# Performance work log

Hardware: AMD Instinct MI355X
Metric: run time of the kernel (lower is better)

## Reference

```python
import jax, jax.numpy as jnp
import numpy as np

EMBED_DIM = 1024
NUM_HEADS = 16
HEAD_DIM = EMBED_DIM // NUM_HEADS


def setup_inputs() -> dict:
    key = jax.random.key(0)
    k1, k2, k3, k4, k5 = jax.random.split(key, 5)
    x = jax.random.normal(k1, (4, 2048, EMBED_DIM), dtype=jnp.float32)
    # nn.Linear params: weight [out, in], bias [out]
    s_in = 1.0 / np.sqrt(EMBED_DIM)
    W_qkv = jax.random.uniform(k2, (3 * EMBED_DIM, EMBED_DIM), jnp.float32, -s_in, s_in)
    b_qkv = jax.random.uniform(k3, (3 * EMBED_DIM,), jnp.float32, -s_in, s_in)
    W_out = jax.random.uniform(k4, (EMBED_DIM, EMBED_DIM), jnp.float32, -s_in, s_in)
    b_out = jax.random.uniform(k5, (EMBED_DIM,), jnp.float32, -s_in, s_in)
    return {"x": x, "W_qkv": W_qkv, "b_qkv": b_qkv, "W_out": W_out, "b_out": b_out}


def reference(x, W_qkv, b_qkv, W_out, b_out):
    B, S, D = x.shape
    H, Dh = NUM_HEADS, HEAD_DIM
    qkv = x @ W_qkv.T + b_qkv                      # [B, S, 3D]
    qkv = qkv.reshape(B, S, 3, H, Dh)
    q = qkv[:, :, 0].transpose(0, 2, 1, 3)        # [B, H, S, Dh]
    k = qkv[:, :, 1].transpose(0, 2, 1, 3)
    v = qkv[:, :, 2].transpose(0, 2, 1, 3)
    scale = 1.0 / jnp.sqrt(jnp.asarray(Dh, x.dtype))
    scores = jnp.einsum('bhqd,bhkd->bhqk', q, k) * scale  # [B, H, S, S]
    attn = jax.nn.softmax(scores, axis=-1)
    out = jnp.einsum('bhqk,bhkd->bhqd', attn, v)  # [B, H, S, Dh]
    out = out.transpose(0, 2, 1, 3).reshape(B, S, D)
    return out @ W_out.T + b_out
```

## Files before the change

kernel.cpp:

```cpp
#include <hip/hip_runtime.h>

#define BB 4
#define SS 2048
#define DD 1024
#define HH 16
#define DHH 64
#define MM (BB*SS)

typedef __bf16 bf16x8 __attribute__((ext_vector_type(8)));
typedef __bf16 bf16x4 __attribute__((ext_vector_type(4)));
typedef float  f32x4  __attribute__((ext_vector_type(4)));
typedef float  f32x16 __attribute__((ext_vector_type(16)));
typedef unsigned int u32;
typedef unsigned int u32x4 __attribute__((ext_vector_type(4)));

__device__ __forceinline__ unsigned short f2bf(float x) {
    unsigned int u = __float_as_uint(x);
    u += 0x7FFFu + ((u >> 16) & 1u);
    return (unsigned short)(u >> 16);
}

__device__ __forceinline__ void glds16(const __bf16* g, __bf16* l) {
    __builtin_amdgcn_global_load_lds(
        (const __attribute__((address_space(1))) void*)g,
        (__attribute__((address_space(3))) void*)l, 16, 0, 0);
}

__global__ __launch_bounds__(256) void cvt_all(
    const float4* __restrict__ x,  const float4* __restrict__ wq,
    const float4* __restrict__ wo,
    ushort4* __restrict__ xb, ushort4* __restrict__ wqb, ushort4* __restrict__ wob)
{
    int i = blockIdx.x * 256 + threadIdx.x;
    const float4* src; ushort4* dst; int j;
    if (i < 2097152)      { src = x;  dst = xb;  j = i; }
    else if (i < 2883584) { src = wq; dst = wqb; j = i - 2097152; }
    else                  { src = wo; dst = wob; j = i - 2883584; }
    float4 v = src[j];
    ushort4 o;
    o.x = f2bf(v.x); o.y = f2bf(v.y); o.z = f2bf(v.z); o.w = f2bf(v.w);
    dst[j] = o;
}

__global__ __launch_bounds__(256) void qkv_gemm(
    const __bf16* __restrict__ A,
    const __bf16* __restrict__ W,
    const float* __restrict__ bias,
    __bf16* __restrict__ Qp,
    __bf16* __restrict__ Kp,
    __bf16* __restrict__ Vp)
{
    __shared__ __bf16 smem[16896];
#define CT(r,c) smem[(r)*132 + (c)]
    __bf16* As = smem;
    __bf16* Bs = smem + 8192;
    const int tid  = threadIdx.x;
    const int m0   = blockIdx.x * 128;
    const int n0   = blockIdx.y * 128;
    const int lane = tid & 63;
    const int wid  = tid >> 6;
    const int fr   = lane & 15;
    const int quad = lane >> 4;
    const int wm   = (wid >> 1) * 64;
    const int wn   = (wid & 1) * 64;

    const int srow = lane >> 3;
    const int sg   = ((lane & 7) - srow) & 7;

    f32x4 acc[4][4] = {};

    for (int k0 = 0; k0 < DD; k0 += 64) {
        __syncthreads();
        #pragma unroll
        for (int p = 0; p < 4; ++p) {
            int cidx = p * 4 + wid;
            int r = cidx * 8 + srow;
            glds16(A + (size_t)(m0 + r) * DD + k0 + sg * 8, As + cidx * 512);
            glds16(W + (size_t)(n0 + r) * DD + k0 + sg * 8, Bs + cidx * 512);
        }
        __syncthreads();

        bf16x8 af[2][4], bw[2][4];
        #pragma unroll
        for (int kc = 0; kc < 2; ++kc)
            #pragma unroll
            for (int t = 0; t < 4; ++t) {
                int col = ((kc * 4 + quad + fr) & 7) * 8;
                af[kc][t] = *(const bf16x8*)&As[(wm + t*16 + fr) * 64 + col];
                bw[kc][t] = *(const bf16x8*)&Bs[(wn + t*16 + fr) * 64 + col];
            }
        #pragma unroll
        for (int kc = 0; kc < 2; ++kc)
            #pragma unroll
            for (int mt = 0; mt < 4; ++mt)
                #pragma unroll
                for (int nt = 0; nt < 4; ++nt)
                    acc[mt][nt] = __builtin_amdgcn_mfma_f32_16x16x32_bf16(
                        af[kc][mt], bw[kc][nt], acc[mt][nt], 0, 0, 0);
    }

    __syncthreads();
    const int t3 = n0 >> 10;
    const int b  = m0 >> 11;
    const int s0 = m0 & (SS - 1);

    float bn[4];
    #pragma unroll
    for (int nt = 0; nt < 4; ++nt) bn[nt] = bias[n0 + wn + nt*16 + fr];

    if (t3 == 2) {
        #pragma unroll
        for (int nt = 0; nt < 4; ++nt)
            #pragma unroll
            for (int mt = 0; mt < 4; ++mt) {
                f32x4 t;
                #pragma unroll
                for (int i = 0; i < 4; ++i) t[i] = acc[mt][nt][i] + bn[nt];
                *(bf16x4*)&CT(wn + nt*16 + fr, wm + mt*16 + quad*4) =
                    __builtin_convertvector(t, bf16x4);
            }
        __syncthreads();
        const int pn0 = n0 - 2048;
        #pragma unroll
        for (int p = 0; p < 8; ++p) {
            int g = tid + p * 256;
            int r = g >> 4;
            int c = (g & 15) << 3;
            int pn = pn0 + r, h = pn >> 6, dh = pn & 63;
            *(uint4*)&Vp[((size_t)((b*HH + h)*DHH + dh))*SS + s0 + c] = *(uint4*)&CT(r, c);
        }
    } else {
        __bf16* dst = (t3 == 0) ? Qp : Kp;
        const float qscale = (t3 == 0) ? 0.125f * 1.44269504088896340736f : 1.0f;
        #pragma unroll
        for (int nt = 0; nt < 4; ++nt)
            #pragma unroll
            for (int mt = 0; mt < 4; ++mt)
                #pragma unroll
                for (int i = 0; i < 4; ++i)
                    CT(wm + mt*16 + quad*4 + i, wn + nt*16 + fr) =
                        (__bf16)((acc[mt][nt][i] + bn[nt]) * qscale);
        __syncthreads();
        const int pn0 = (t3 == 0) ? n0 : n0 - 1024;
        #pragma unroll
        for (int p = 0; p < 8; ++p) {
            int g = tid + p * 256;
            int r = g >> 4;
            int c = (g & 15) << 3;
            int pn = pn0 + c, h = pn >> 6, dh = pn & 63;
            *(uint4*)&dst[((size_t)((b*HH + h))*SS + s0 + r)*DHH + dh] = *(uint4*)&CT(r, c);
        }
    }
#undef CT
}

__global__ __launch_bounds__(256) void out_gemm(
    const __bf16* __restrict__ A,
    const __bf16* __restrict__ W,
    const float* __restrict__ bias,
    float* __restrict__ out)
{
    __shared__ __bf16 smem[16384];
    __bf16* As = smem;
    __bf16* Bs = smem + 8192;
    const int tid  = threadIdx.x;
    const int m0   = blockIdx.x * 128;
    const int n0   = blockIdx.y * 128;
    const int lane = tid & 63;
    const int wid  = tid >> 6;
    const int fr   = lane & 15;
    const int quad = lane >> 4;
    const int wm   = (wid >> 1) * 64;
    const int wn   = (wid & 1) * 64;

    const int srow = lane >> 3;
    const int sg   = ((lane & 7) - srow) & 7;

    f32x4 acc[4][4] = {};

    for (int k0 = 0; k0 < DD; k0 += 64) {
        __syncthreads();
        #pragma unroll
        for (int p = 0; p < 4; ++p) {
            int cidx = p * 4 + wid;
            int r = cidx * 8 + srow;
            glds16(A + (size_t)(m0 + r) * DD + k0 + sg * 8, As + cidx * 512);
            glds16(W + (size_t)(n0 + r) * DD + k0 + sg * 8, Bs + cidx * 512);
        }
        __syncthreads();

        bf16x8 af[2][4], bw[2][4];
        #pragma unroll
        for (int kc = 0; kc < 2; ++kc)
            #pragma unroll
            for (int t = 0; t < 4; ++t) {
                int col = ((kc * 4 + quad + fr) & 7) * 8;
                af[kc][t] = *(const bf16x8*)&As[(wm + t*16 + fr) * 64 + col];
                bw[kc][t] = *(const bf16x8*)&Bs[(wn + t*16 + fr) * 64 + col];
            }
        #pragma unroll
        for (int kc = 0; kc < 2; ++kc)
            #pragma unroll
            for (int mt = 0; mt < 4; ++mt)
                #pragma unroll
                for (int nt = 0; nt < 4; ++nt)
                    acc[mt][nt] = __builtin_amdgcn_mfma_f32_16x16x32_bf16(
                        af[kc][mt], bw[kc][nt], acc[mt][nt], 0, 0, 0);
    }

    #pragma unroll
    for (int nt = 0; nt < 4; ++nt) {
        int n  = n0 + wn + nt*16 + fr;
        float bnv = bias[n];
        #pragma unroll
        for (int mt = 0; mt < 4; ++mt) {
            #pragma unroll
            for (int i = 0; i < 4; ++i) {
                int m = m0 + wm + mt*16 + quad*4 + i;
                out[(size_t)m * DD + n] = acc[mt][nt][i] + bnv;
            }
        }
    }
}

__global__ __launch_bounds__(256, 2) void attn_mfma(
    const __bf16* __restrict__ Qp,
    const __bf16* __restrict__ Kp,
    const __bf16* __restrict__ Vp,
    __bf16* __restrict__ Op)
{
    __shared__ __bf16 Ks[2][64 * 64];
    __shared__ __bf16 VT[2][64 * 64];
    __shared__ __bf16 Ps[256][72];
    __shared__ float  Ls[256];

    const int tid  = threadIdx.x;
    const int q0   = blockIdx.x * 256;
    const int bh   = blockIdx.y;
    const size_t base = (size_t)bh * SS * DHH;
    const int lane = tid & 63;
    const int wid  = tid >> 6;
    const int c32  = lane & 31;
    const int hi   = lane >> 5;
    const int wrow = wid * 64;

    const int srow = lane >> 3;
    const int sg   = ((lane & 7) - srow) & 7;

#define STAGE_KV(buf, kt_)                                                        \
    {                                                                             \
        _Pragma("unroll")                                                         \
        for (int p = 0; p < 2; ++p) {                                             \
            int cidx = p * 4 + wid;                  \
            int r = cidx * 8 + srow;                                              \
            glds16(Kp + base + (size_t)((kt_) + r) * DHH + sg * 8,                \
                   &Ks[buf][cidx * 512]);                                         \
            glds16(Vp + base + (size_t)r * SS + (kt_) + sg * 8,                   \
                   &VT[buf][cidx * 512]);                                         \
        }                                                                         \
    }

    bf16x8 bq[2][4];
    #pragma unroll
    for (int qt = 0; qt < 2; ++qt)
        #pragma unroll
        for (int ks = 0; ks < 4; ++ks)
            bq[qt][ks] = *(const bf16x8*)
                (Qp + base + (size_t)(q0 + wrow + qt*32 + c32) * DHH + ks*16 + hi*8);

    f32x16 o[2][2] = {};
    float lp[2] = {};

    STAGE_KV(0, 0)
    __syncthreads();

    int cur = 0;
    for (int kt = 0; kt < SS; kt += 64) {
        if (kt + 64 < SS) STAGE_KV(cur ^ 1, kt + 64)
        const __bf16* Kc = Ks[cur];
        const __bf16* Vc = VT[cur];

        u32 pw[2][2][8];

        #pragma unroll
        for (int kt2 = 0; kt2 < 2; ++kt2) {
            bf16x8 bk[4];
            #pragma unroll
            for (int ks = 0; ks < 4; ++ks)
                bk[ks] = *(const bf16x8*)
                    &Kc[(kt2*32 + c32) * 64 + ((ks*2 + hi + c32) & 7) * 8];
            #pragma unroll
            for (int qt = 0; qt < 2; ++qt) {
                f32x16 s = {};
                __builtin_amdgcn_s_setprio(1);
                #pragma unroll
                for (int ks = 0; ks < 4; ++ks)
                    s = __builtin_amdgcn_mfma_f32_32x32x16_bf16(
                        bk[ks], bq[qt][ks], s, 0, 0, 0);
                __builtin_amdgcn_s_setprio(0);
                #pragma unroll
                for (int e = 0; e < 16; ++e) s[e] = __builtin_amdgcn_exp2f(s[e]);
                lp[qt] += ((s[0]+s[1])+(s[2]+s[3])) + ((s[4]+s[5])+(s[6]+s[7]))
                        + ((s[8]+s[9])+(s[10]+s[11])) + ((s[12]+s[13])+(s[14]+s[15]));
                #pragma unroll
                for (int kk = 0; kk < 2; ++kk) {
                    u32 wa, wb, wc, wd;
                    asm("v_cvt_pk_bf16_f32 %0, %1, %2" : "=v"(wa) : "v"(s[kk*8+0]), "v"(s[kk*8+1]));
                    asm("v_cvt_pk_bf16_f32 %0, %1, %2" : "=v"(wb) : "v"(s[kk*8+4]), "v"(s[kk*8+5]));
                    asm("v_cvt_pk_bf16_f32 %0, %1, %2" : "=v"(wc) : "v"(s[kk*8+2]), "v"(s[kk*8+3]));
                    asm("v_cvt_pk_bf16_f32 %0, %1, %2" : "=v"(wd) : "v"(s[kk*8+6]), "v"(s[kk*8+7]));
                    asm("v_permlane32_swap_b32 %0, %1" : "+v"(wa), "+v"(wb));
                    asm("v_permlane32_swap_b32 %0, %1" : "+v"(wc), "+v"(wd));
                    pw[qt][kt2][kk*4+0] = wa;
                    pw[qt][kt2][kk*4+1] = wc;
                    pw[qt][kt2][kk*4+2] = wb;
                    pw[qt][kt2][kk*4+3] = wd;
                }
            }
        }

        #pragma unroll
        for (int ks = 0; ks < 4; ++ks) {
            const int kt2 = ks >> 1, kk = ks & 1;
            bf16x8 bv[2];
            #pragma unroll
            for (int dt = 0; dt < 2; ++dt)
                bv[dt] = *(const bf16x8*)
                    &Vc[(dt*32 + c32) * 64 + ((ks*2 + hi + c32) & 7) * 8];
            __builtin_amdgcn_s_setprio(1);
            #pragma unroll
            for (int qt = 0; qt < 2; ++qt) {
                u32x4 t = { pw[qt][kt2][kk*4+0], pw[qt][kt2][kk*4+1],
                            pw[qt][kt2][kk*4+2], pw[qt][kt2][kk*4+3] };
                bf16x8 pa = __builtin_bit_cast(bf16x8, t);
                #pragma unroll
                for (int dt = 0; dt < 2; ++dt)
                    o[qt][dt] = __builtin_amdgcn_mfma_f32_32x32x16_bf16(
                        pa, bv[dt], o[qt][dt], 0, 0, 0);
            }
            __builtin_amdgcn_s_setprio(0);
        }

        __syncthreads();
        cur ^= 1;
    }
#undef STAGE_KV

    #pragma unroll
    for (int qt = 0; qt < 2; ++qt) {
        float v = lp[qt] + __shfl_xor(lp[qt], 32);
        Ls[wrow + qt*32 + c32] = v;
    }

    #pragma unroll
    for (int qt = 0; qt < 2; ++qt)
        #pragma unroll
        for (int r = 0; r < 16; ++r) {
            int row = wrow + qt*32 + (r & 3) + 8*(r >> 2) + 4*hi;
            float inv = 1.0f / Ls[row];
            #pragma unroll
            for (int dt = 0; dt < 2; ++dt)
                Ps[row][dt*32 + c32] = (__bf16)(o[qt][dt][r] * inv);
        }
    __syncthreads();

    const int b = bh >> 4, h = bh & (HH - 1);
    #pragma unroll
    for (int p = 0; p < 8; ++p) {
        int g = tid + p * 256;
        int r = g >> 3;
        int c = (g & 7) << 3;
        *(uint4*)&Op[((size_t)(b*SS + q0 + r))*DD + h*DHH + c] = *(uint4*)&Ps[r][c];
    }
}


extern "C" void kernel_launch(void* const* d_in, const int* in_sizes, int n_in,
                              void* d_out, int out_size, void* d_ws, size_t ws_size,
                              hipStream_t stream)
{
    const float* x     = (const float*)d_in[0];
    const float* W_qkv = (const float*)d_in[1];
    const float* b_qkv = (const float*)d_in[2];
    const float* W_out = (const float*)d_in[3];
    const float* b_out = (const float*)d_in[4];
    float* out = (float*)d_out;

    __bf16* ws  = (__bf16*)d_ws;
    __bf16* xb  = ws;
    __bf16* wqb = xb  + (size_t)8388608;
    __bf16* wob = wqb + (size_t)3145728;
    __bf16* qp  = wob + (size_t)1048576;
    __bf16* kp  = qp  + (size_t)8388608;
    __bf16* vp  = kp  + (size_t)8388608;
    __bf16* op  = vp  + (size_t)8388608;

    cvt_all<<<12288, 256, 0, stream>>>(
        (const float4*)x, (const float4*)W_qkv, (const float4*)W_out,
        (ushort4*)xb, (ushort4*)wqb, (ushort4*)wob);

    qkv_gemm<<<dim3(MM/128, 3*DD/128), 256, 0, stream>>>(xb, wqb, b_qkv, qp, kp, vp);
    attn_mfma<<<dim3(SS/256, BB*HH), 256, 0, stream>>>(qp, kp, vp, op);
    out_gemm<<<dim3(MM/128, DD/128), 256, 0, stream>>>(op, wob, b_out, out);
}
```

Measured before the change: 264.1 us.

## Split attention block into 8 waves of 32 query rows and alias LDS

The attention kernel now launches 512 threads per block, each wave owning 32 query rows instead of 64. This halves per-wave accumulator and P registers and targets 4 blocks per CU. K/V staging is spread across 8 waves with one load each. The P output buffer is aliased onto the K/V staging LDS region to shrink shared memory per block. The cost is that each K/V tile loaded into LDS now feeds less MFMA work per wave, and more waves contend at each barrier.

```diff
diff --git a/kernel.cpp b/kernel.cpp
--- a/kernel.cpp
+++ b/kernel.cpp
@@ -223,16 +223,17 @@
     }
 }
 
-__global__ __launch_bounds__(256, 2) void attn_mfma(
+__global__ __launch_bounds__(512, 4) void attn_mfma(
     const __bf16* __restrict__ Qp,
     const __bf16* __restrict__ Kp,
     const __bf16* __restrict__ Vp,
     __bf16* __restrict__ Op)
 {
-    __shared__ __bf16 Ks[2][64 * 64];
-    __shared__ __bf16 VT[2][64 * 64];
-    __shared__ __bf16 Ps[256][72];
-    __shared__ float  Ls[256];
+    __shared__ __align__(16) char smem[37888];
+    __bf16* const KsB = (__bf16*)smem;
+    __bf16* const VTB = (__bf16*)(smem + 16384);
+    float*  const Ls  = (float*)(smem + 36864);
+#define PS(r,c) (((__bf16*)smem)[(r)*72 + (c)])
 
     const int tid  = threadIdx.x;
     const int q0   = blockIdx.x * 256;
@@ -242,34 +243,28 @@
     const int wid  = tid >> 6;
     const int c32  = lane & 31;
     const int hi   = lane >> 5;
-    const int wrow = wid * 64;
+    const int wrow = wid * 32;
 
     const int srow = lane >> 3;
     const int sg   = ((lane & 7) - srow) & 7;
 
 #define STAGE_KV(buf, kt_)                                                        \
     {                                                                             \
-        _Pragma("unroll")                                                         \
-        for (int p = 0; p < 2; ++p) {                                             \
-            int cidx = p * 4 + wid;                  \
-            int r = cidx * 8 + srow;                                              \
-            glds16(Kp + base + (size_t)((kt_) + r) * DHH + sg * 8,                \
-                   &Ks[buf][cidx * 512]);                                         \
-            glds16(Vp + base + (size_t)r * SS + (kt_) + sg * 8,                   \
-                   &VT[buf][cidx * 512]);                                         \
-        }                                                                         \
-    }
-
-    bf16x8 bq[2][4];
-    #pragma unroll
-    for (int qt = 0; qt < 2; ++qt)
-        #pragma unroll
-        for (int ks = 0; ks < 4; ++ks)
-            bq[qt][ks] = *(const bf16x8*)
-                (Qp + base + (size_t)(q0 + wrow + qt*32 + c32) * DHH + ks*16 + hi*8);
-
-    f32x16 o[2][2] = {};
-    float lp[2] = {};
+        int r = wid * 8 + srow;                                                   \
+        glds16(Kp + base + (size_t)((kt_) + r) * DHH + sg * 8,                    \
+               KsB + (buf) * 4096 + wid * 512);                                   \
+        glds16(Vp + base + (size_t)r * SS + (kt_) + sg * 8,                       \
+               VTB + (buf) * 4096 + wid * 512);                                   \
+    }
+
+    bf16x8 bq[4];
+    #pragma unroll
+    for (int ks = 0; ks < 4; ++ks)
+        bq[ks] = *(const bf16x8*)
+            (Qp + base + (size_t)(q0 + wrow + c32) * DHH + ks*16 + hi*8);
+
+    f32x16 o[2] = {};
+    float lp = 0.0f;
 
     STAGE_KV(0, 0)
     __syncthreads();
@@ -277,10 +272,10 @@
     int cur = 0;
     for (int kt = 0; kt < SS; kt += 64) {
         if (kt + 64 < SS) STAGE_KV(cur ^ 1, kt + 64)
-        const __bf16* Kc = Ks[cur];
-        const __bf16* Vc = VT[cur];
-
-        u32 pw[2][2][8];
+        const __bf16* Kc = KsB + cur * 4096;
+        const __bf16* Vc = VTB + cur * 4096;
+
+        u32 pw[2][8];
 
         #pragma unroll
         for (int kt2 = 0; kt2 < 2; ++kt2) {
@@ -289,33 +284,30 @@
             for (int ks = 0; ks < 4; ++ks)
                 bk[ks] = *(const bf16x8*)
                     &Kc[(kt2*32 + c32) * 64 + ((ks*2 + hi + c32) & 7) * 8];
-            #pragma unroll
-            for (int qt = 0; qt < 2; ++qt) {
-                f32x16 s = {};
-                __builtin_amdgcn_s_setprio(1);
-                #pragma unroll
-                for (int ks = 0; ks < 4; ++ks)
-                    s = __builtin_amdgcn_mfma_f32_32x32x16_bf16(
-                        bk[ks], bq[qt][ks], s, 0, 0, 0);
-                __builtin_amdgcn_s_setprio(0);
-                #pragma unroll
-                for (int e = 0; e < 16; ++e) s[e] = __builtin_amdgcn_exp2f(s[e]);
-                lp[qt] += ((s[0]+s[1])+(s[2]+s[3])) + ((s[4]+s[5])+(s[6]+s[7]))
-                        + ((s[8]+s[9])+(s[10]+s[11])) + ((s[12]+s[13])+(s[14]+s[15]));
-                #pragma unroll
-                for (int kk = 0; kk < 2; ++kk) {
-                    u32 wa, wb, wc, wd;
-                    asm("v_cvt_pk_bf16_f32 %0, %1, %2" : "=v"(wa) : "v"(s[kk*8+0]), "v"(s[kk*8+1]));
-                    asm("v_cvt_pk_bf16_f32 %0, %1, %2" : "=v"(wb) : "v"(s[kk*8+4]), "v"(s[kk*8+5]));
-                    asm("v_cvt_pk_bf16_f32 %0, %1, %2" : "=v"(wc) : "v"(s[kk*8+2]), "v"(s[kk*8+3]));
-                    asm("v_cvt_pk_bf16_f32 %0, %1, %2" : "=v"(wd) : "v"(s[kk*8+6]), "v"(s[kk*8+7]));
-                    asm("v_permlane32_swap_b32 %0, %1" : "+v"(wa), "+v"(wb));
-                    asm("v_permlane32_swap_b32 %0, %1" : "+v"(wc), "+v"(wd));
-                    pw[qt][kt2][kk*4+0] = wa;
-                    pw[qt][kt2][kk*4+1] = wc;
-                    pw[qt][kt2][kk*4+2] = wb;
-                    pw[qt][kt2][kk*4+3] = wd;
-                }
+            f32x16 s = {};
+            __builtin_amdgcn_s_setprio(1);
+            #pragma unroll
+            for (int ks = 0; ks < 4; ++ks)
+                s = __builtin_amdgcn_mfma_f32_32x32x16_bf16(
+                    bk[ks], bq[ks], s, 0, 0, 0);
+            __builtin_amdgcn_s_setprio(0);
+            #pragma unroll
+            for (int e = 0; e < 16; ++e) s[e] = __builtin_amdgcn_exp2f(s[e]);
+            lp += ((s[0]+s[1])+(s[2]+s[3])) + ((s[4]+s[5])+(s[6]+s[7]))
+                + ((s[8]+s[9])+(s[10]+s[11])) + ((s[12]+s[13])+(s[14]+s[15]));
+            #pragma unroll
+            for (int kk = 0; kk < 2; ++kk) {
+                u32 wa, wb, wc, wd;
+                asm("v_cvt_pk_bf16_f32 %0, %1, %2" : "=v"(wa) : "v"(s[kk*8+0]), "v"(s[kk*8+1]));
+                asm("v_cvt_pk_bf16_f32 %0, %1, %2" : "=v"(wb) : "v"(s[kk*8+4]), "v"(s[kk*8+5]));
+                asm("v_cvt_pk_bf16_f32 %0, %1, %2" : "=v"(wc) : "v"(s[kk*8+2]), "v"(s[kk*8+3]));
+                asm("v_cvt_pk_bf16_f32 %0, %1, %2" : "=v"(wd) : "v"(s[kk*8+6]), "v"(s[kk*8+7]));
+                asm("v_permlane32_swap_b32 %0, %1" : "+v"(wa), "+v"(wb));
+                asm("v_permlane32_swap_b32 %0, %1" : "+v"(wc), "+v"(wd));
+                pw[kt2][kk*4+0] = wa;
+                pw[kt2][kk*4+1] = wc;
+                pw[kt2][kk*4+2] = wb;
+                pw[kt2][kk*4+3] = wd;
             }
         }
 
@@ -327,17 +319,14 @@
             for (int dt = 0; dt < 2; ++dt)
                 bv[dt] = *(const bf16x8*)
                     &Vc[(dt*32 + c32) * 64 + ((ks*2 + hi + c32) & 7) * 8];
+            u32x4 t = { pw[kt2][kk*4+0], pw[kt2][kk*4+1],
+                        pw[kt2][kk*4+2], pw[kt2][kk*4+3] };
+            bf16x8 pa = __builtin_bit_cast(bf16x8, t);
             __builtin_amdgcn_s_setprio(1);
             #pragma unroll
-            for (int qt = 0; qt < 2; ++qt) {
-                u32x4 t = { pw[qt][kt2][kk*4+0], pw[qt][kt2][kk*4+1],
-                            pw[qt][kt2][kk*4+2], pw[qt][kt2][kk*4+3] };
-                bf16x8 pa = __builtin_bit_cast(bf16x8, t);
-                #pragma unroll
-                for (int dt = 0; dt < 2; ++dt)
-                    o[qt][dt] = __builtin_amdgcn_mfma_f32_32x32x16_bf16(
-                        pa, bv[dt], o[qt][dt], 0, 0, 0);
-            }
+            for (int dt = 0; dt < 2; ++dt)
+                o[dt] = __builtin_amdgcn_mfma_f32_32x32x16_bf16(
+                    pa, bv[dt], o[dt], 0, 0, 0);
             __builtin_amdgcn_s_setprio(0);
         }
 
@@ -346,32 +335,30 @@
     }
 #undef STAGE_KV
 
-    #pragma unroll
-    for (int qt = 0; qt < 2; ++qt) {
-        float v = lp[qt] + __shfl_xor(lp[qt], 32);
-        Ls[wrow + qt*32 + c32] = v;
-    }
-
-    #pragma unroll
-    for (int qt = 0; qt < 2; ++qt)
-        #pragma unroll
-        for (int r = 0; r < 16; ++r) {
-            int row = wrow + qt*32 + (r & 3) + 8*(r >> 2) + 4*hi;
-            float inv = 1.0f / Ls[row];
-            #pragma unroll
-            for (int dt = 0; dt < 2; ++dt)
-                Ps[row][dt*32 + c32] = (__bf16)(o[qt][dt][r] * inv);
-        }
+    {
+        float v = lp + __shfl_xor(lp, 32);
+        Ls[wrow + c32] = v;
+    }
+
+    #pragma unroll
+    for (int r = 0; r < 16; ++r) {
+        int row = wrow + (r & 3) + 8*(r >> 2) + 4*hi;
+        float inv = 1.0f / Ls[row];
+        #pragma unroll
+        for (int dt = 0; dt < 2; ++dt)
+            PS(row, dt*32 + c32) = (__bf16)(o[dt][r] * inv);
+    }
     __syncthreads();
 
     const int b = bh >> 4, h = bh & (HH - 1);
     #pragma unroll
-    for (int p = 0; p < 8; ++p) {
-        int g = tid + p * 256;
+    for (int p = 0; p < 4; ++p) {
+        int g = tid + p * 512;
         int r = g >> 3;
         int c = (g & 7) << 3;
-        *(uint4*)&Op[((size_t)(b*SS + q0 + r))*DD + h*DHH + c] = *(uint4*)&Ps[r][c];
-    }
+        *(uint4*)&Op[((size_t)(b*SS + q0 + r))*DD + h*DHH + c] = *(uint4*)&PS(r, c);
+    }
+#undef PS
 }
 
 
@@ -400,6 +387,6 @@
         (ushort4*)xb, (ushort4*)wqb, (ushort4*)wob);
 
     qkv_gemm<<<dim3(MM/128, 3*DD/128), 256, 0, stream>>>(xb, wqb, b_qkv, qp, kp, vp);
-    attn_mfma<<<dim3(SS/256, BB*HH), 256, 0, stream>>>(qp, kp, vp, op);
+    attn_mfma<<<dim3(SS/256, BB*HH), 512, 0, stream>>>(qp, kp, vp, op);
     out_gemm<<<dim3(MM/128, DD/128), 256, 0, stream>>>(op, wob, b_out, out);
 }
```

Result: no change. 264.4 us (+0.1%).

## Remap workgroups per XCD for L2 locality and alias attention LDS buffers

Applied to the files above, without the earlier changes.

Switches all three compute kernels to 1D grids and remaps block IDs so that consecutive workgroups dispatched round-robin to the same XCD share A rows (GEMMs) or the same batch-head (attention), aiming to improve per-XCD L2 reuse. The attention kernel also overlays the output staging buffer Ps onto the K/V double buffers, shrinking LDS from about 73KB to 37KB, which could allow more resident blocks per CU. The aliasing relies on the final barrier ordering before Ps writes, and the mapping assumes the specific grid sizes.

```diff
diff --git a/kernel.cpp b/kernel.cpp
--- a/kernel.cpp
+++ b/kernel.cpp
@@ -55,8 +55,11 @@
     __bf16* As = smem;
     __bf16* Bs = smem + 8192;
     const int tid  = threadIdx.x;
-    const int m0   = blockIdx.x * 128;
-    const int n0   = blockIdx.y * 128;
+    const int wg   = blockIdx.x;
+    const int xcd  = wg & 7;
+    const int slot = wg >> 3;
+    const int m0   = (xcd * 8 + (slot & 7)) * 128;
+    const int n0   = (slot >> 3) * 128;
     const int lane = tid & 63;
     const int wid  = tid >> 6;
     const int fr   = lane & 15;
@@ -164,8 +167,11 @@
     __bf16* As = smem;
     __bf16* Bs = smem + 8192;
     const int tid  = threadIdx.x;
-    const int m0   = blockIdx.x * 128;
-    const int n0   = blockIdx.y * 128;
+    const int wg   = blockIdx.x;
+    const int xcd  = wg & 7;
+    const int slot = wg >> 3;
+    const int m0   = (xcd * 8 + (slot & 7)) * 128;
+    const int n0   = (slot >> 3) * 128;
     const int lane = tid & 63;
     const int wid  = tid >> 6;
     const int fr   = lane & 15;
@@ -229,14 +235,18 @@
     const __bf16* __restrict__ Vp,
     __bf16* __restrict__ Op)
 {
-    __shared__ __bf16 Ks[2][64 * 64];
-    __shared__ __bf16 VT[2][64 * 64];
-    __shared__ __bf16 Ps[256][72];
-    __shared__ float  Ls[256];
+    __shared__ __align__(16) char smem[37888];
+    __bf16* const KsB = (__bf16*)smem;
+    __bf16* const VTB = (__bf16*)(smem + 16384);
+    float*  const Ls  = (float*)(smem + 36864);
+#define PS(r,c) (((__bf16*)smem)[(r)*72 + (c)])
 
     const int tid  = threadIdx.x;
-    const int q0   = blockIdx.x * 256;
-    const int bh   = blockIdx.y;
+    const int wg   = blockIdx.x;
+    const int xcd  = wg & 7;
+    const int slot = wg >> 3;
+    const int bh   = xcd * 8 + (slot >> 3);
+    const int q0   = (slot & 7) * 256;
     const size_t base = (size_t)bh * SS * DHH;
     const int lane = tid & 63;
     const int wid  = tid >> 6;
@@ -254,9 +264,9 @@
             int cidx = p * 4 + wid;                  \
             int r = cidx * 8 + srow;                                              \
             glds16(Kp + base + (size_t)((kt_) + r) * DHH + sg * 8,                \
-                   &Ks[buf][cidx * 512]);                                         \
+                   KsB + (buf) * 4096 + cidx * 512);                              \
             glds16(Vp + base + (size_t)r * SS + (kt_) + sg * 8,                   \
-                   &VT[buf][cidx * 512]);                                         \
+                   VTB + (buf) * 4096 + cidx * 512);                              \
         }                                                                         \
     }
 
@@ -277,8 +287,8 @@
     int cur = 0;
     for (int kt = 0; kt < SS; kt += 64) {
         if (kt + 64 < SS) STAGE_KV(cur ^ 1, kt + 64)
-        const __bf16* Kc = Ks[cur];
-        const __bf16* Vc = VT[cur];
+        const __bf16* Kc = KsB + cur * 4096;
+        const __bf16* Vc = VTB + cur * 4096;
 
         u32 pw[2][2][8];
 
@@ -360,7 +370,7 @@
             float inv = 1.0f / Ls[row];
             #pragma unroll
             for (int dt = 0; dt < 2; ++dt)
-                Ps[row][dt*32 + c32] = (__bf16)(o[qt][dt][r] * inv);
+                PS(row, dt*32 + c32) = (__bf16)(o[qt][dt][r] * inv);
         }
     __syncthreads();
 
@@ -370,8 +380,9 @@
         int g = tid + p * 256;
         int r = g >> 3;
         int c = (g & 7) << 3;
-        *(uint4*)&Op[((size_t)(b*SS + q0 + r))*DD + h*DHH + c] = *(uint4*)&Ps[r][c];
-    }
+        *(uint4*)&Op[((size_t)(b*SS + q0 + r))*DD + h*DHH + c] = *(uint4*)&PS(r, c);
+    }
+#undef PS
 }
 
 
@@ -399,7 +410,7 @@
         (const float4*)x, (const float4*)W_qkv, (const float4*)W_out,
         (ushort4*)xb, (ushort4*)wqb, (ushort4*)wob);
 
-    qkv_gemm<<<dim3(MM/128, 3*DD/128), 256, 0, stream>>>(xb, wqb, b_qkv, qp, kp, vp);
-    attn_mfma<<<dim3(SS/256, BB*HH), 256, 0, stream>>>(qp, kp, vp, op);
-    out_gemm<<<dim3(MM/128, DD/128), 256, 0, stream>>>(op, wob, b_out, out);
-}
+    qkv_gemm<<<1536, 256, 0, stream>>>(xb, wqb, b_qkv, qp, kp, vp);
+    attn_mfma<<<512, 256, 0, stream>>>(qp, kp, vp, op);
+    out_gemm<<<512, 256, 0, stream>>>(op, wob, b_out, out);
+}
```

After: 261.2 us. No clear change (-1.1%).
